# Kernel optimization log

Hardware: AMD Instinct MI355X
Metric: run time of the kernel (lower is better)

The kernel has to match this reference:

```python
import jax, jax.numpy as jnp
import numpy as np

B, KL, XL, DIM, H, PB = 4, 128, 4096, 256, 8, 8
HD = DIM // H
SCALE = HD ** -0.5
N_DIS = 64 + 2


def setup_inputs() -> dict:
    key = jax.random.key(0)
    ks = jax.random.split(key, 10)
    x = jax.random.normal(ks[0], (B, XL, DIM), jnp.float32)
    kernal = jax.random.normal(ks[1], (B, KL, DIM), jnp.float32)
    rd = jax.random.randint(ks[2], (B, KL, XL), 0, N_DIS)
    polar_pos = jax.random.randint(ks[3], (B, KL, XL), 0, PB)
    att_mask = jax.random.uniform(ks[4], (B, H, XL, KL)) < 0.1
    W_qkv = jax.random.normal(ks[5], (DIM, 3 * DIM), jnp.float32) * 0.02
    dis_embed = jax.random.normal(ks[6], (N_DIS, H), jnp.float32) * 0.02
    polar_emb = jax.random.normal(ks[7], (PB, 1), jnp.float32) * 0.02
    W_proj = jax.random.normal(ks[8], (DIM, DIM), jnp.float32) * 0.02
    b_proj = jnp.zeros((DIM,), jnp.float32)
    return dict(x=x, kernal=kernal, rd=rd, polar_pos=polar_pos, att_mask=att_mask,
                W_qkv=W_qkv, dis_embed=dis_embed, polar_emb=polar_emb,
                W_proj=W_proj, b_proj=b_proj)


def _heads(t, h):
    b, n, d = t.shape
    return t.reshape(b, n, h, d // h).transpose(0, 2, 1, 3)  # b h n hd


def reference(x, kernal, rd, polar_pos, att_mask, W_qkv, dis_embed, polar_emb, W_proj, b_proj):
    b, xl, dim = x.shape
    kl = kernal.shape[1]
    h = H
    scale = (dim // h) ** -0.5

    q, k, v = [_heads(t, h) for t in jnp.split(x @ W_qkv, 3, axis=-1)]        # b h xl hd
    k_q, k_k, k_v = [_heads(t, h) for t in jnp.split(kernal @ W_qkv, 3, axis=-1)]  # b h kl hd

    rd_e = dis_embed[rd].transpose(0, 3, 1, 2)  # (b,kl,xl,h) -> (b,h,kl,xl)

    # kernel -> x attention scores
    k_x_attn = jnp.einsum('bhkd,bhxd->bhkx', k_q, k) * scale  # b h kl xl

    # main orientation: one-hot-weighted |attn| reduced over x, argmax over polar bins
    pp = jnp.broadcast_to(polar_pos[:, None], (b, h, kl, xl))  # b h kl xl
    polar_hot = jax.nn.one_hot(pp, PB, dtype=k_x_attn.dtype)   # b h kl xl o
    ori_sum = jnp.einsum('bhkx,bhkxo->bhko', jnp.abs(k_x_attn), polar_hot)
    main_ori = jnp.argmax(ori_sum, axis=-1)                    # b h kl
    new_polar = pp - main_ori[..., None]
    new_polar = jnp.where(new_polar < 0, new_polar + PB, new_polar)
    polar_bias = polar_emb[new_polar, 0]                       # b h kl xl

    mask_k = att_mask.transpose(0, 1, 3, 2)                    # b h kl xl
    k_x_attn = jnp.where(mask_k, jnp.asarray(-1e6, k_x_attn.dtype), k_x_attn)
    attn_k = jax.nn.softmax(k_x_attn + rd_e + polar_bias, axis=-1)
    k_out = jnp.einsum('bhkx,bhxd->bhkd', attn_k, v)
    k_out = k_out.transpose(0, 2, 1, 3).reshape(b, kl, dim) @ W_proj + b_proj

    # x -> kernel attention scores
    x_k_attn = jnp.einsum('bhxd,bhkd->bhxk', q, k_k) * scale   # b h xl kl
    x_k_attn = jnp.where(att_mask, jnp.asarray(-1e9, x_k_attn.dtype), x_k_attn)
    x_k_attn = jax.nn.softmax(x_k_attn + rd_e.transpose(0, 1, 3, 2)
                              + polar_bias.transpose(0, 1, 3, 2), axis=-1)
    x_out = jnp.einsum('bhxk,bhkd->bhxd', x_k_attn, k_v)
    x_out = x_out.transpose(0, 2, 1, 3).reshape(b, xl, dim) @ W_proj + b_proj

    return (x_out, k_out)
```

## Files before the change

kernel.cpp:

```cpp
#include <hip/hip_runtime.h>
#include <hip/hip_bf16.h>

#define B_    4
#define KL_   128
#define XL_   4096
#define DIM_  256
#define H_    8
#define HD_   32
#define PB_   8
#define NDIS_ 66
#define TDIM_ 768
#define SCALE_ 0.17677669529663687f
#define NS_   4
#define XCH_  (XL_ / NS_)
#define NCH2_ 64
#define KC2_  16

#define NB_CVT_  4096
#define NB_PACK_ 2048
#define NB_WQ_   768
#define NB_WP_   256

typedef float v4f __attribute__((ext_vector_type(4)));
typedef short v8s __attribute__((ext_vector_type(8)));

__device__ __forceinline__ unsigned short f2bf(float f) {
    __hip_bfloat16 h = __float2bfloat16(f);
    return __builtin_bit_cast(unsigned short, h);
}
__device__ __forceinline__ float bf2f(unsigned short u) {
    return __bfloat162float(__builtin_bit_cast(__hip_bfloat16, u));
}
__device__ __forceinline__ void cvt_hilo(float v, unsigned short& hi, unsigned short& lo) {
    hi = f2bf(v);
    lo = f2bf(v - bf2f(hi));
}

__global__ __launch_bounds__(256) void preamble(const float* __restrict__ x,
                                                const int* __restrict__ att_mask,
                                                const float* __restrict__ W_qkv,
                                                const float* __restrict__ W_proj,
                                                unsigned short* __restrict__ xh,
                                                unsigned short* __restrict__ xl,
                                                unsigned int* __restrict__ mbits,
                                                unsigned short* __restrict__ wqh,
                                                unsigned short* __restrict__ wql,
                                                unsigned short* __restrict__ wph,
                                                unsigned short* __restrict__ wpl) {
    const int bid = blockIdx.x, tid = threadIdx.x;
    if (bid < NB_CVT_) {
        size_t i = (size_t)bid * 256 + tid;
        float4 v = *(const float4*)&x[i * 4];
        ushort4 h, l;
        cvt_hilo(v.x, h.x, l.x);
        cvt_hilo(v.y, h.y, l.y);
        cvt_hilo(v.z, h.z, l.z);
        cvt_hilo(v.w, h.w, l.w);
        *(ushort4*)&xh[i * 4] = h;
        *(ushort4*)&xl[i * 4] = l;
    } else if (bid < NB_CVT_ + NB_PACK_) {
        size_t wid = (size_t)(bid - NB_CVT_) * 256 + tid;
        const int* src = &att_mask[wid * 32];
        unsigned bits = 0;
#pragma unroll
        for (int i = 0; i < 8; ++i) {
            int4 m4 = *(const int4*)&src[i * 4];
            bits |= (m4.x ? 1u : 0u) << (i * 4 + 0);
            bits |= (m4.y ? 1u : 0u) << (i * 4 + 1);
            bits |= (m4.z ? 1u : 0u) << (i * 4 + 2);
            bits |= (m4.w ? 1u : 0u) << (i * 4 + 3);
        }
        mbits[wid] = bits;
    } else if (bid < NB_CVT_ + NB_PACK_ + NB_WQ_) {
        int n = bid - (NB_CVT_ + NB_PACK_), k = tid;
        float v = W_qkv[(size_t)k * TDIM_ + n];
        unsigned short h, l;
        cvt_hilo(v, h, l);
        wqh[(size_t)n * DIM_ + k] = h;
        wql[(size_t)n * DIM_ + k] = l;
    } else {
        int n = bid - (NB_CVT_ + NB_PACK_ + NB_WQ_), k = tid;
        float v = W_proj[(size_t)k * DIM_ + n];
        unsigned short h, l;
        cvt_hilo(v, h, l);
        wph[(size_t)n * DIM_ + k] = h;
        wpl[(size_t)n * DIM_ + k] = l;
    }
}

__global__ __launch_bounds__(256) void gemm_mfma(const unsigned short* __restrict__ Ah,
                                                 const unsigned short* __restrict__ Al,
                                                 const unsigned short* __restrict__ Bh,
                                                 const unsigned short* __restrict__ Bl,
                                                 float* __restrict__ C,
                                                 const float* __restrict__ bias,
                                                 int M, int N, int K, int mode,
                                                 unsigned short* __restrict__ qh,
                                                 unsigned short* __restrict__ kh,
                                                 unsigned short* __restrict__ kl2,
                                                 float* __restrict__ vx) {
    __shared__ __align__(16) unsigned short Ah_s[128 * 32];
    __shared__ __align__(16) unsigned short Al_s[128 * 32];
    __shared__ __align__(16) unsigned short Bh_s[128 * 32];
    __shared__ __align__(16) unsigned short Bl_s[128 * 32];
    const int tid = threadIdx.x;
    const int w = tid >> 6, lane = tid & 63;
    const int c = lane & 15, q = lane >> 4;
    const int bm = blockIdx.y * 128, bn = blockIdx.x * 128;

    const int lrow = lane >> 2;
    const int lcol = (lane & 3) * 8;

    v4f acc[2][8] = {};
    for (int k0 = 0; k0 < K; k0 += 32) {
        __syncthreads();
#pragma unroll
        for (int i = 0; i < 2; ++i) {
            const int chunk = w * 2 + i;
            const int row = chunk * 16 + lrow;
            const size_t ga = (size_t)(bm + row) * K + k0 + lcol;
            const size_t gb = (size_t)(bn + row) * K + k0 + lcol;
            const int lo = chunk * 512;
            __builtin_amdgcn_global_load_lds(
                (const __attribute__((address_space(1))) unsigned int*)&Ah[ga],
                (__attribute__((address_space(3))) unsigned int*)&Ah_s[lo], 16, 0, 0);
            __builtin_amdgcn_global_load_lds(
                (const __attribute__((address_space(1))) unsigned int*)&Al[ga],
                (__attribute__((address_space(3))) unsigned int*)&Al_s[lo], 16, 0, 0);
            __builtin_amdgcn_global_load_lds(
                (const __attribute__((address_space(1))) unsigned int*)&Bh[gb],
                (__attribute__((address_space(3))) unsigned int*)&Bh_s[lo], 16, 0, 0);
            __builtin_amdgcn_global_load_lds(
                (const __attribute__((address_space(1))) unsigned int*)&Bl[gb],
                (__attribute__((address_space(3))) unsigned int*)&Bl_s[lo], 16, 0, 0);
        }
        asm volatile("s_waitcnt vmcnt(0)" ::: "memory");
        __syncthreads();
        v8s afh[2], afl[2];
#pragma unroll
        for (int mt = 0; mt < 2; ++mt) {
            afh[mt] = *(v8s*)&Ah_s[(w * 32 + mt * 16 + c) * 32 + q * 8];
            afl[mt] = *(v8s*)&Al_s[(w * 32 + mt * 16 + c) * 32 + q * 8];
        }
#pragma unroll
        for (int nt = 0; nt < 8; ++nt) {
            v8s bfh = *(v8s*)&Bh_s[(nt * 16 + c) * 32 + q * 8];
            v8s bfl = *(v8s*)&Bl_s[(nt * 16 + c) * 32 + q * 8];
#pragma unroll
            for (int mt = 0; mt < 2; ++mt) {
                acc[mt][nt] = __builtin_amdgcn_mfma_f32_16x16x32_bf16(afl[mt], bfh, acc[mt][nt], 0, 0, 0);
                acc[mt][nt] = __builtin_amdgcn_mfma_f32_16x16x32_bf16(afh[mt], bfl, acc[mt][nt], 0, 0, 0);
                acc[mt][nt] = __builtin_amdgcn_mfma_f32_16x16x32_bf16(afh[mt], bfh, acc[mt][nt], 0, 0, 0);
            }
        }
    }
    if (mode == 0) {
#pragma unroll
        for (int mt = 0; mt < 2; ++mt) {
#pragma unroll
            for (int nt = 0; nt < 8; ++nt) {
                int col = bn + nt * 16 + c;
                float bv = bias ? bias[col] : 0.0f;
#pragma unroll
                for (int r = 0; r < 4; ++r) {
                    int row = bm + w * 32 + mt * 16 + q * 4 + r;
                    C[(size_t)row * N + col] = acc[mt][nt][r] + bv;
                }
            }
        }
    } else {
#pragma unroll
        for (int mt = 0; mt < 2; ++mt) {
#pragma unroll
            for (int nt = 0; nt < 8; ++nt) {
                int col = bn + nt * 16 + c;
#pragma unroll
                for (int r = 0; r < 4; ++r) {
                    int row = bm + w * 32 + mt * 16 + q * 4 + r;
                    float v = acc[mt][nt][r];
                    if (col < DIM_) {
                        qh[(size_t)row * DIM_ + col] = f2bf(v);
                    } else if (col < 2 * DIM_) {
                        unsigned short hi, lo;
                        cvt_hilo(v, hi, lo);
                        kh[(size_t)row * DIM_ + col - DIM_] = hi;
                        kl2[(size_t)row * DIM_ + col - DIM_] = lo;
                    } else {
                        vx[(size_t)row * DIM_ + col - 2 * DIM_] = v;
                    }
                }
            }
        }
    }
}

__global__ __launch_bounds__(256) void gemm64(const float* __restrict__ A,
                                              const float* __restrict__ Bw,
                                              float* __restrict__ C,
                                              const float* __restrict__ bias,
                                              int M, int N, int K) {
    __shared__ __align__(16) float As[16][68];
    __shared__ __align__(16) float Bs[16][64];
    const int tid = threadIdx.x;
    const int tx = tid & 15, ty = tid >> 4;
    const int bn = blockIdx.x * 64, bm = blockIdx.y * 64;
    const int am = tid >> 2, ac = tid & 3;
    float acc[4][4] = {};
    for (int k0 = 0; k0 < K; k0 += 16) {
        float4 a4 = *(const float4*)&A[(size_t)(bm + am) * K + k0 + ac * 4];
        As[ac * 4 + 0][am] = a4.x;
        As[ac * 4 + 1][am] = a4.y;
        As[ac * 4 + 2][am] = a4.z;
        As[ac * 4 + 3][am] = a4.w;
        *(float4*)&Bs[ty][tx * 4] = *(const float4*)&Bw[(size_t)(k0 + ty) * N + bn + tx * 4];
        __syncthreads();
#pragma unroll
        for (int kk = 0; kk < 16; ++kk) {
            float4 av = *(const float4*)&As[kk][ty * 4];
            float4 bv = *(const float4*)&Bs[kk][tx * 4];
            float a[4] = {av.x, av.y, av.z, av.w};
            float b[4] = {bv.x, bv.y, bv.z, bv.w};
#pragma unroll
            for (int i = 0; i < 4; ++i)
#pragma unroll
                for (int j = 0; j < 4; ++j) acc[i][j] += a[i] * b[j];
        }
        __syncthreads();
    }
#pragma unroll
    for (int i = 0; i < 4; ++i) {
        int m = bm + ty * 4 + i;
#pragma unroll
        for (int j = 0; j < 4; ++j) {
            int n = bn + tx * 4 + j;
            float v = acc[i][j];
            if (bias) v += bias[n];
            C[(size_t)m * N + n] = v;
        }
    }
}

__global__ __launch_bounds__(256) void gemm64_qkv(const float* __restrict__ A,
                                                  const float* __restrict__ Bw,
                                                  unsigned short* __restrict__ Kqh,
                                                  unsigned short* __restrict__ Kql,
                                                  unsigned short* __restrict__ Kk_bf,
                                                  unsigned short* __restrict__ VT_bf,
                                                  int M, int N, int K) {
    __shared__ __align__(16) float As[16][68];
    __shared__ __align__(16) float Bs[16][64];
    const int tid = threadIdx.x;
    const int tx = tid & 15, ty = tid >> 4;
    const int bn = blockIdx.x * 64, bm = blockIdx.y * 64;
    const int am = tid >> 2, ac = tid & 3;
    float acc[4][4] = {};
    for (int k0 = 0; k0 < K; k0 += 16) {
        float4 a4 = *(const float4*)&A[(size_t)(bm + am) * K + k0 + ac * 4];
        As[ac * 4 + 0][am] = a4.x;
        As[ac * 4 + 1][am] = a4.y;
        As[ac * 4 + 2][am] = a4.z;
        As[ac * 4 + 3][am] = a4.w;
        *(float4*)&Bs[ty][tx * 4] = *(const float4*)&Bw[(size_t)(k0 + ty) * N + bn + tx * 4];
        __syncthreads();
#pragma unroll
        for (int kk = 0; kk < 16; ++kk) {
            float4 av = *(const float4*)&As[kk][ty * 4];
            float4 bv = *(const float4*)&Bs[kk][tx * 4];
            float a[4] = {av.x, av.y, av.z, av.w};
            float b[4] = {bv.x, bv.y, bv.z, bv.w};
#pragma unroll
            for (int i = 0; i < 4; ++i)
#pragma unroll
                for (int j = 0; j < 4; ++j) acc[i][j] += a[i] * b[j];
        }
        __syncthreads();
    }
#pragma unroll
    for (int i = 0; i < 4; ++i) {
        int m = bm + ty * 4 + i;
        int b = m >> 7, k = m & 127;
#pragma unroll
        for (int j = 0; j < 4; ++j) {
            int n = bn + tx * 4 + j;
            float v = acc[i][j];
            if (n < DIM_) {
                unsigned short hi, lo;
                cvt_hilo(v, hi, lo);
                int h = n >> 5, d = n & 31;
                size_t o = ((size_t)(b * H_ + h) * KL_ + k) * HD_ + d;
                Kqh[o] = hi;
                Kql[o] = lo;
            } else if (n < 2 * DIM_) {
                int nn = n - DIM_, h = nn >> 5, d = nn & 31;
                Kk_bf[((size_t)(b * H_ + h) * KL_ + k) * HD_ + d] = f2bf(v);
            } else {
                int nn = n - 2 * DIM_, h = nn >> 5, d = nn & 31;
                VT_bf[((size_t)(b * H_ + h) * HD_ + d) * KL_ + k] = f2bf(v);
            }
        }
    }
}

__global__ __launch_bounds__(256) void score_bins_mfma4(const unsigned short* __restrict__ kxh,
                                                        const unsigned short* __restrict__ kxl,
                                                        const unsigned short* __restrict__ Kqh_g,
                                                        const unsigned short* __restrict__ Kql_g,
                                                        const int* __restrict__ rd,
                                                        const int* __restrict__ polar_pos,
                                                        const unsigned int* __restrict__ mbits,
                                                        const float* __restrict__ dis_embed,
                                                        __hip_bfloat16* __restrict__ Sg,
                                                        float* __restrict__ binspart) {
    const int b = blockIdx.z, h = blockIdx.y, xc = blockIdx.x;
    const int x0 = xc * 64;
    const int tid = threadIdx.x;
    const int w = tid >> 6, lane = tid & 63;
    const int c15 = lane & 15, q = lane >> 4;
    const size_t bh = (size_t)(b * H_ + h);

    __shared__ unsigned int mskb[64][5];
    __shared__ float de_h[NDIS_];
    __shared__ float binsL[8][4][16][PB_ + 1];
    __shared__ __align__(16) unsigned short Ss[2][16][72];

    {
        int xr = tid >> 2, kg = tid & 3;
        mskb[xr][kg] = mbits[(bh * XL_ + x0 + xr) * 4 + kg];
    }
    if (tid < NDIS_) de_h[tid] = dis_embed[tid * H_ + h];
    __syncthreads();

    v8s axh, axl;
    {
        const size_t aoff = ((size_t)b * XL_ + x0 + w * 16 + c15) * DIM_ + h * HD_ + q * 8;
        axh = *(const v8s*)&kxh[aoff];
        axl = *(const v8s*)&kxl[aoff];
    }

    v8s bqh[2], bql[2];
    int4 r4[2], p4[2];
    auto load_nt = [&](int nt, int s) {
        const int k = nt * 16 + c15;
        const size_t kqoff = (bh * KL_ + k) * HD_ + q * 8;
        bqh[s] = *(const v8s*)&Kqh_g[kqoff];
        bql[s] = *(const v8s*)&Kql_g[kqoff];
        const size_t rowoff = ((size_t)(b * KL_ + k)) * XL_ + x0 + w * 16 + q * 4;
        r4[s] = *(const int4*)&rd[rowoff];
        p4[s] = *(const int4*)&polar_pos[rowoff];
    };
    load_nt(0, 0);

#pragma unroll
    for (int nt = 0; nt < 8; ++nt) {
        const int s = nt & 1;
        if (nt < 7) load_nt(nt + 1, s ^ 1);

        const int k = nt * 16 + c15;
        v4f D = {0.f, 0.f, 0.f, 0.f};
        D = __builtin_amdgcn_mfma_f32_16x16x32_bf16(axl, bqh[s], D, 0, 0, 0);
        D = __builtin_amdgcn_mfma_f32_16x16x32_bf16(axh, bql[s], D, 0, 0, 0);
        D = __builtin_amdgcn_mfma_f32_16x16x32_bf16(axh, bqh[s], D, 0, 0, 0);

        float bins[PB_] = {};
        {
            int rv[4] = {r4[s].x, r4[s].y, r4[s].z, r4[s].w};
            int pv[4] = {p4[s].x, p4[s].y, p4[s].z, p4[s].w};
            ushort4 pack;
#pragma unroll
            for (int r = 0; r < 4; ++r) {
                float sc = D[r] * SCALE_;
                float a = fabsf(sc);
                int pp = pv[r];
#pragma unroll
                for (int pb = 0; pb < PB_; ++pb) bins[pb] += (pp == pb) ? a : 0.0f;
                int xloc = w * 16 + q * 4 + r;
                int mbit = (mskb[xloc][k >> 5] >> (k & 31)) & 1;
                float sp = (mbit ? -1e6f : sc) + de_h[rv[r]];
                ((unsigned short*)&pack)[r] = f2bf(sp);
            }
            *(ushort4*)&Ss[s][c15][w * 16 + q * 4] = pack;
        }

#pragma unroll
        for (int pb = 0; pb < PB_; ++pb) {
            bins[pb] += __shfl_xor(bins[pb], 16);
            bins[pb] += __shfl_xor(bins[pb], 32);
        }
        if (q == 0) {
#pragma unroll
            for (int pb = 0; pb < PB_; ++pb) binsL[nt][w][c15][pb] = bins[pb];
        }

        __syncthreads();
        {
            int row = tid >> 4, seg = tid & 15;
            unsigned short* dst = (unsigned short*)Sg +
                (bh * KL_ + nt * 16 + row) * XL_ + x0 + seg * 4;
            *(uint2*)dst = *(const uint2*)&Ss[s][row][seg * 4];
        }
    }
    __syncthreads();
    {
        int k = tid >> 1, half = tid & 1;
        int nt = k >> 4, c = k & 15;
        float4 s = {0.f, 0.f, 0.f, 0.f};
#pragma unroll
        for (int w4 = 0; w4 < 4; ++w4) {
            const float* bp = &binsL[nt][w4][c][half * 4];
            s.x += bp[0]; s.y += bp[1]; s.z += bp[2]; s.w += bp[3];
        }
        *(float4*)&binspart[(bh * KL_ + k) * (NCH2_ * PB_) + xc * PB_ + half * 4] = s;
    }
}

__global__ __launch_bounds__(256) void bins_argmax(const float* __restrict__ binspart,
                                                   int* __restrict__ main_ori) {
    const int w = threadIdx.x >> 6, lane = threadIdx.x & 63;
    const int row = blockIdx.x * 4 + w;
    float s[PB_];
#pragma unroll
    for (int pb = 0; pb < PB_; ++pb) s[pb] = 0.0f;
    if (lane < NCH2_) {
        const float* bp = &binspart[(size_t)row * (NCH2_ * PB_) + lane * PB_];
#pragma unroll
        for (int pb = 0; pb < PB_; ++pb) s[pb] = bp[pb];
    }
#pragma unroll
    for (int m = 1; m < 64; m <<= 1)
#pragma unroll
        for (int pb = 0; pb < PB_; ++pb) s[pb] += __shfl_xor(s[pb], m);
    if (lane == 0) {
        float best = s[0];
        int bi = 0;
#pragma unroll
        for (int pb = 1; pb < PB_; ++pb)
            if (s[pb] > best) { best = s[pb]; bi = pb; }
        main_ori[row] = bi;
    }
}

__global__ __launch_bounds__(256) void flash_cached2(const float* __restrict__ vx,
                                                     const __hip_bfloat16* __restrict__ Sg,
                                                     const int* __restrict__ polar_pos,
                                                     const float* __restrict__ polar_emb,
                                                     const int* __restrict__ main_ori,
                                                     float* __restrict__ part) {
    const int b = blockIdx.z, h = blockIdx.y;
    const int kch = blockIdx.x / NS_, xc = blockIdx.x % NS_;
    const int k0 = kch * KC2_;
    const int tid = threadIdx.x;
    const int ki = tid >> 4, xt = tid & 15;

    __shared__ __align__(16) float4 vs[64][9];
    __shared__ int pol_s[KC2_][68];
    __shared__ float pe[PB_];

    if (tid < PB_) pe[tid] = polar_emb[tid];
    const size_t bh = (size_t)(b * H_ + h);
    const size_t row_k = bh * KL_ + k0 + ki;
    const int mo = main_ori[row_k];
    const int xbeg = xc * XCH_;

    float l = 0.f;
    float4 acc[8] = {};
    __syncthreads();
    for (int t = 0; t < XCH_ / 64; ++t) {
        const int x0 = xbeg + t * 64;
        __syncthreads();
#pragma unroll
        for (int i = 0; i < 2; ++i) {
            int id = tid + 256 * i;
            int row = id >> 3, c = id & 7;
            vs[row][c] = *(const float4*)&vx[(size_t)(b * XL_ + x0 + row) * DIM_ + h * HD_ + c * 4];
        }
        {
            int kk = tid >> 4, c = tid & 15;
            *(int4*)&pol_s[kk][c * 4] =
                *(const int4*)&polar_pos[(size_t)(b * KL_ + k0 + kk) * XL_ + x0 + c * 4];
        }
        __syncthreads();
#pragma unroll
        for (int j = 0; j < 4; ++j) {
            int xl = xt + 16 * j;
            int x = x0 + xl;
            float sp = __bfloat162float(Sg[row_k * XL_ + x]);
            int pp = pol_s[ki][xl];
            int np = pp - mo;
            np += (np >> 31) & PB_;
            float p = __expf(sp + pe[np]);
            l += p;
#pragma unroll
            for (int c = 0; c < 8; ++c) {
                float4 v = vs[xl][c];
                acc[c].x += p * v.x; acc[c].y += p * v.y;
                acc[c].z += p * v.z; acc[c].w += p * v.w;
            }
        }
    }
#pragma unroll
    for (int m = 1; m < 16; m <<= 1) {
        l += __shfl_xor(l, m, 16);
#pragma unroll
        for (int c = 0; c < 8; ++c) {
            acc[c].x += __shfl_xor(acc[c].x, m, 16);
            acc[c].y += __shfl_xor(acc[c].y, m, 16);
            acc[c].z += __shfl_xor(acc[c].z, m, 16);
            acc[c].w += __shfl_xor(acc[c].w, m, 16);
        }
    }
    if (xt == 0) {
        float* dst = &part[(size_t)(row_k * NS_ + xc) * 36];
#pragma unroll
        for (int c = 0; c < 8; ++c) *(float4*)&dst[c * 4] = acc[c];
        dst[32] = l;
    }
}

__global__ __launch_bounds__(256) void merge_cached(const float* __restrict__ part,
                                                    float* __restrict__ kout_pre) {
    const int tid = threadIdx.x;
    const int ri = tid >> 5, d = tid & 31;
    const int row = blockIdx.x * 8 + ri;
    float l = 0.f, a = 0.f;
#pragma unroll
    for (int c = 0; c < NS_; ++c) {
        const float* p = &part[(size_t)(row * NS_ + c) * 36];
        l += p[32];
        a += p[d];
    }
    int k = row & (KL_ - 1);
    int bh = row >> 7;
    int h = bh & (H_ - 1), b = bh >> 3;
    kout_pre[(size_t)(b * KL_ + k) * DIM_ + h * HD_ + d] = a / l;
}

__global__ __launch_bounds__(256) void attn_x_mfma(const unsigned short* __restrict__ qxh,
                                                   const unsigned short* __restrict__ Kk_bf,
                                                   const unsigned short* __restrict__ VT_bf,
                                                   const int* __restrict__ rd,
                                                   const int* __restrict__ polar_pos,
                                                   const unsigned int* __restrict__ mbits,
                                                   const float* __restrict__ dis_embed,
                                                   const float* __restrict__ polar_emb,
                                                   const int* __restrict__ main_ori,
                                                   unsigned short* __restrict__ oh,
                                                   unsigned short* __restrict__ ol) {
    const int b = blockIdx.z, h = blockIdx.y;
    const int x0 = blockIdx.x * 64;
    const int tid = threadIdx.x;
    const int wave = tid >> 6, lane = tid & 63;
    const int c = lane & 15, q = lane >> 4;

    __shared__ __align__(16) unsigned short P_s[4][16][136];
    __shared__ unsigned short rp_s[KL_][72];
    __shared__ unsigned int msk_s[64][5];
    __shared__ float de_h[NDIS_];
    __shared__ float pe[PB_];
    __shared__ int mo_s[KL_];

    const size_t bh = (size_t)(b * H_ + h);
    if (tid < NDIS_) de_h[tid] = dis_embed[tid * H_ + h];
    if (tid < PB_) pe[tid] = polar_emb[tid];
    if (tid < KL_) mo_s[tid] = main_ori[bh * KL_ + tid];
    {
        int xr = tid >> 2, kg = tid & 3;
        msk_s[xr][kg] = mbits[(bh * XL_ + x0 + xr) * 4 + kg];
    }
    __syncthreads();

#pragma unroll
    for (int i = 0; i < 8; ++i) {
        int id = tid + 256 * i;
        int k = id >> 4, cc = id & 15;
        size_t gb = (size_t)(b * KL_ + k) * XL_ + x0 + cc * 4;
        int4 r4 = *(const int4*)&rd[gb];
        int4 p4 = *(const int4*)&polar_pos[gb];
        int mo = mo_s[k];
        int n0 = p4.x - mo; n0 += (n0 >> 31) & PB_;
        int n1 = p4.y - mo; n1 += (n1 >> 31) & PB_;
        int n2 = p4.z - mo; n2 += (n2 >> 31) & PB_;
        int n3 = p4.w - mo; n3 += (n3 >> 31) & PB_;
        rp_s[k][cc * 4 + 0] = (unsigned short)(r4.x | (n0 << 8));
        rp_s[k][cc * 4 + 1] = (unsigned short)(r4.y | (n1 << 8));
        rp_s[k][cc * 4 + 2] = (unsigned short)(r4.z | (n2 << 8));
        rp_s[k][cc * 4 + 3] = (unsigned short)(r4.w | (n3 << 8));
    }
    __syncthreads();

    v8s aq = *(const v8s*)&qxh[(size_t)(b * XL_ + x0 + wave * 16 + c) * DIM_ + h * HD_ + q * 8];

    const unsigned short* KkB = &Kk_bf[(size_t)bh * KL_ * HD_];
    v4f S[8];
#pragma unroll
    for (int t = 0; t < 8; ++t) {
        v8s bk = *(const v8s*)&KkB[(size_t)(t * 16 + c) * HD_ + q * 8];
        S[t] = __builtin_amdgcn_mfma_f32_16x16x32_bf16(aq, bk, (v4f){0.f, 0.f, 0.f, 0.f}, 0, 0, 0);
    }

    const int xloc = wave * 16;
    float lr[4] = {0.f, 0.f, 0.f, 0.f};
#pragma unroll
    for (int t = 0; t < 8; ++t) {
#pragma unroll
        for (int r = 0; r < 4; ++r) {
            int krow = t * 16 + c;
            int xrow = q * 4 + r;
            unsigned short rp = rp_s[krow][xloc + xrow];
            int mbit = (msk_s[xloc + xrow][krow >> 5] >> (krow & 31)) & 1;
            float sval = S[t][r] * SCALE_;
            float tval = (mbit ? -25.0f : sval) + de_h[rp & 0x7f] + pe[(rp >> 8) & 7];
            float p = __expf(tval);
            unsigned short pb = f2bf(p);
            P_s[wave][xrow][krow] = pb;
            lr[r] += bf2f(pb);
        }
    }
#pragma unroll
    for (int r = 0; r < 4; ++r) {
#pragma unroll
        for (int m = 1; m < 16; m <<= 1) lr[r] += __shfl_xor(lr[r], m);
    }
    __syncthreads();

    const unsigned short* VTB = &VT_bf[(size_t)bh * HD_ * KL_];
    v4f O0 = {0.f, 0.f, 0.f, 0.f}, O1 = {0.f, 0.f, 0.f, 0.f};
#pragma unroll
    for (int kc = 0; kc < 4; ++kc) {
        v8s ap = *(v8s*)&P_s[wave][c][kc * 32 + q * 8];
        v8s bv0 = *(const v8s*)&VTB[(size_t)c * KL_ + kc * 32 + q * 8];
        v8s bv1 = *(const v8s*)&VTB[(size_t)(16 + c) * KL_ + kc * 32 + q * 8];
        O0 = __builtin_amdgcn_mfma_f32_16x16x32_bf16(ap, bv0, O0, 0, 0, 0);
        O1 = __builtin_amdgcn_mfma_f32_16x16x32_bf16(ap, bv1, O1, 0, 0, 0);
    }

#pragma unroll
    for (int r = 0; r < 4; ++r) {
        int xg = x0 + wave * 16 + q * 4 + r;
        float inv = 1.0f / lr[r];
        size_t obase = (size_t)(b * XL_ + xg) * DIM_ + h * HD_;
        float v0 = O0[r] * inv;
        float v1 = O1[r] * inv;
        unsigned short h0, l0, h1, l1;
        cvt_hilo(v0, h0, l0);
        cvt_hilo(v1, h1, l1);
        oh[obase + c] = h0;
        ol[obase + c] = l0;
        oh[obase + 16 + c] = h1;
        ol[obase + 16 + c] = l1;
    }
}

extern "C" void kernel_launch(void* const* d_in, const int* in_sizes, int n_in,
                              void* d_out, int out_size, void* d_ws, size_t ws_size,
                              hipStream_t stream) {
    const float* x         = (const float*)d_in[0];
    const float* kernal    = (const float*)d_in[1];
    const int* rd          = (const int*)d_in[2];
    const int* polar_pos   = (const int*)d_in[3];
    const int* att_mask    = (const int*)d_in[4];
    const float* W_qkv     = (const float*)d_in[5];
    const float* dis_embed = (const float*)d_in[6];
    const float* polar_emb = (const float*)d_in[7];
    const float* W_proj    = (const float*)d_in[8];
    const float* b_proj    = (const float*)d_in[9];
    float* out             = (float*)d_out;

    char* base = (char*)d_ws;
    size_t off = 0;
    auto alloc = [&](size_t bytes) { void* p = base + off; off = (off + bytes + 255) & ~255ULL; return p; };
    const size_t MX = (size_t)B_ * XL_;

    float* vx        = (float*)alloc(MX * DIM_ * 4);
    unsigned short* qxh = (unsigned short*)alloc(MX * DIM_ * 2);
    unsigned short* kxh = (unsigned short*)alloc(MX * DIM_ * 2);
    unsigned short* kxl = (unsigned short*)alloc(MX * DIM_ * 2);
    float* binspart  = (float*)alloc((size_t)B_ * H_ * KL_ * NCH2_ * PB_ * 4);
    float* kout_pre  = (float*)alloc((size_t)B_ * KL_ * DIM_ * 4);
    int* main_ori    = (int*)alloc(B_ * H_ * KL_ * 4);
    float* part      = (float*)alloc((size_t)B_ * H_ * KL_ * NS_ * 36 * 4);
    __hip_bfloat16* Sg = (__hip_bfloat16*)alloc((size_t)B_ * H_ * KL_ * XL_ * 2);
    unsigned short* wph = (unsigned short*)alloc((size_t)DIM_ * DIM_ * 2);
    unsigned short* wpl = (unsigned short*)alloc((size_t)DIM_ * DIM_ * 2);
    unsigned short* wqh = (unsigned short*)alloc((size_t)TDIM_ * DIM_ * 2);
    unsigned short* wql = (unsigned short*)alloc((size_t)TDIM_ * DIM_ * 2);
    unsigned int* mbits = (unsigned int*)alloc((size_t)B_ * H_ * XL_ * (KL_ / 32) * 4);
    unsigned short* Kqh_g = (unsigned short*)alloc((size_t)B_ * H_ * KL_ * HD_ * 2);
    unsigned short* Kql_g = (unsigned short*)alloc((size_t)B_ * H_ * KL_ * HD_ * 2);
    unsigned short* Kk_bf = (unsigned short*)alloc((size_t)B_ * H_ * KL_ * HD_ * 2);
    unsigned short* VT_bf = (unsigned short*)alloc((size_t)B_ * H_ * HD_ * KL_ * 2);

    unsigned short* xh = (unsigned short*)Sg;
    unsigned short* xl_ = xh + MX * DIM_;
    unsigned short* oh = (unsigned short*)Sg;
    unsigned short* ol = oh + MX * DIM_;

    preamble<<<dim3(NB_CVT_ + NB_PACK_ + NB_WQ_ + NB_WP_), 256, 0, stream>>>(
        x, att_mask, W_qkv, W_proj, xh, xl_, mbits, wqh, wql, wph, wpl);

    gemm_mfma<<<dim3(TDIM_ / 128, MX / 128), 256, 0, stream>>>(
        xh, xl_, wqh, wql, nullptr, nullptr, MX, TDIM_, DIM_, 1, qxh, kxh, kxl, vx);
    gemm64_qkv<<<dim3(TDIM_ / 64, (B_ * KL_) / 64), 256, 0, stream>>>(
        kernal, W_qkv, Kqh_g, Kql_g, Kk_bf, VT_bf, B_ * KL_, TDIM_, DIM_);

    score_bins_mfma4<<<dim3(NCH2_, H_, B_), 256, 0, stream>>>(
        kxh, kxl, Kqh_g, Kql_g, rd, polar_pos, mbits, dis_embed, Sg, binspart);
    bins_argmax<<<dim3(B_ * H_ * KL_ / 4), 256, 0, stream>>>(binspart, main_ori);
    flash_cached2<<<dim3((KL_ / KC2_) * NS_, H_, B_), 256, 0, stream>>>(
        vx, Sg, polar_pos, polar_emb, main_ori, part);
    merge_cached<<<dim3(B_ * H_ * KL_ / 8), 256, 0, stream>>>(part, kout_pre);

    attn_x_mfma<<<dim3(XL_ / 64, H_, B_), 256, 0, stream>>>(
        qxh, Kk_bf, VT_bf, rd, polar_pos, mbits, dis_embed, polar_emb, main_ori, oh, ol);

    gemm_mfma<<<dim3(DIM_ / 128, MX / 128), 256, 0, stream>>>(
        oh, ol, wph, wpl, out, b_proj, MX, DIM_, DIM_, 0, nullptr, nullptr, nullptr, nullptr);
    gemm64<<<dim3(DIM_ / 64, (B_ * KL_) / 64), 256, 0, stream>>>(
        kout_pre, W_proj, out + (size_t)B_ * XL_ * DIM_, b_proj, B_ * KL_, DIM_, DIM_);
}
```

Measured before the change: 335.7 us.

## Stage QKV GEMM epilogue through LDS for vectorized bf16 stores and remap blocks per XCD

The bf16 outputs of the QKV projection GEMM (q, and k split into high and low parts) are now staged through a padded LDS scratch tile so each thread writes 16-byte vectors instead of scattered 2-byte stores. The block-column range also selects the epilogue branch directly, where before every element tested its column. The grid becomes one-dimensional with a remap that keeps consecutive row tiles on the same XCD, aiming at better L2 reuse of shared operands. This adds extra barriers and LDS traffic to the epilogue.

```diff
diff --git a/kernel.cpp b/kernel.cpp
--- a/kernel.cpp
+++ b/kernel.cpp
@@ -15,6 +15,7 @@
 #define XCH_  (XL_ / NS_)
 #define NCH2_ 64
 #define KC2_  16
+#define GM_PITCH_ 132
 
 #define NB_CVT_  4096
 #define NB_PACK_ 2048
@@ -99,14 +100,22 @@
                                                  unsigned short* __restrict__ kh,
                                                  unsigned short* __restrict__ kl2,
                                                  float* __restrict__ vx) {
-    __shared__ __align__(16) unsigned short Ah_s[128 * 32];
-    __shared__ __align__(16) unsigned short Al_s[128 * 32];
-    __shared__ __align__(16) unsigned short Bh_s[128 * 32];
-    __shared__ __align__(16) unsigned short Bl_s[128 * 32];
+    __shared__ __align__(16) char SMEM[64 * GM_PITCH_ * 4];
+    unsigned short* Ah_s = (unsigned short*)SMEM;
+    unsigned short* Al_s = Ah_s + 4096;
+    unsigned short* Bh_s = Ah_s + 8192;
+    unsigned short* Bl_s = Ah_s + 12288;
+    float* scratch = (float*)SMEM;
+
     const int tid = threadIdx.x;
     const int w = tid >> 6, lane = tid & 63;
     const int c = lane & 15, q = lane >> 4;
-    const int bm = blockIdx.y * 128, bn = blockIdx.x * 128;
+
+    const int NBX = N >> 7;
+    const int id = blockIdx.x;
+    const int xcd = id & 7, grp = id >> 3;
+    const int bm = ((grp / NBX) * 8 + xcd) * 128;
+    const int bn = (grp % NBX) * 128;
 
     const int lrow = lane >> 2;
     const int lcol = (lane & 3) * 8;
@@ -168,27 +177,50 @@
                 }
             }
         }
-    } else {
+    } else if (bn >= 2 * DIM_) {
 #pragma unroll
         for (int mt = 0; mt < 2; ++mt) {
 #pragma unroll
             for (int nt = 0; nt < 8; ++nt) {
-                int col = bn + nt * 16 + c;
+                int col = bn + nt * 16 + c - 2 * DIM_;
 #pragma unroll
                 for (int r = 0; r < 4; ++r) {
                     int row = bm + w * 32 + mt * 16 + q * 4 + r;
-                    float v = acc[mt][nt][r];
-                    if (col < DIM_) {
-                        qh[(size_t)row * DIM_ + col] = f2bf(v);
-                    } else if (col < 2 * DIM_) {
-                        unsigned short hi, lo;
-                        cvt_hilo(v, hi, lo);
-                        kh[(size_t)row * DIM_ + col - DIM_] = hi;
-                        kl2[(size_t)row * DIM_ + col - DIM_] = lo;
-                    } else {
-                        vx[(size_t)row * DIM_ + col - 2 * DIM_] = v;
-                    }
+                    vx[(size_t)row * DIM_ + col] = acc[mt][nt][r];
                 }
+            }
+        }
+    } else {
+        for (int mt = 0; mt < 2; ++mt) {
+            __syncthreads();
+#pragma unroll
+            for (int nt = 0; nt < 8; ++nt)
+#pragma unroll
+                for (int r = 0; r < 4; ++r)
+                    scratch[(w * 16 + q * 4 + r) * GM_PITCH_ + nt * 16 + c] = acc[mt][nt][r];
+            __syncthreads();
+            const int or_ = tid & 63, oc = (tid >> 6) * 32;
+            const int grow = bm + (or_ >> 4) * 32 + mt * 16 + (or_ & 15);
+            const float* src = &scratch[or_ * GM_PITCH_ + oc];
+            if (bn < DIM_) {
+                unsigned short tmp[32];
+#pragma unroll
+                for (int j = 0; j < 32; ++j) tmp[j] = f2bf(src[j]);
+                unsigned short* dst = &qh[(size_t)grow * DIM_ + bn + oc];
+#pragma unroll
+                for (int j4 = 0; j4 < 4; ++j4)
+                    *(uint4*)&dst[j4 * 8] = *(uint4*)&tmp[j4 * 8];
+            } else {
+                unsigned short th[32], tl[32];
+#pragma unroll
+                for (int j = 0; j < 32; ++j) cvt_hilo(src[j], th[j], tl[j]);
+                const size_t o = (size_t)grow * DIM_ + bn - DIM_ + oc;
+#pragma unroll
+                for (int j4 = 0; j4 < 4; ++j4)
+                    *(uint4*)&kh[o + j4 * 8] = *(uint4*)&th[j4 * 8];
+#pragma unroll
+                for (int j4 = 0; j4 < 4; ++j4)
+                    *(uint4*)&kl2[o + j4 * 8] = *(uint4*)&tl[j4 * 8];
             }
         }
     }
@@ -697,7 +729,7 @@
     preamble<<<dim3(NB_CVT_ + NB_PACK_ + NB_WQ_ + NB_WP_), 256, 0, stream>>>(
         x, att_mask, W_qkv, W_proj, xh, xl_, mbits, wqh, wql, wph, wpl);
 
-    gemm_mfma<<<dim3(TDIM_ / 128, MX / 128), 256, 0, stream>>>(
+    gemm_mfma<<<dim3((TDIM_ / 128) * (MX / 128)), 256, 0, stream>>>(
         xh, xl_, wqh, wql, nullptr, nullptr, MX, TDIM_, DIM_, 1, qxh, kxh, kxl, vx);
     gemm64_qkv<<<dim3(TDIM_ / 64, (B_ * KL_) / 64), 256, 0, stream>>>(
         kernal, W_qkv, Kqh_g, Kql_g, Kk_bf, VT_bf, B_ * KL_, TDIM_, DIM_);
@@ -712,7 +744,7 @@
     attn_x_mfma<<<dim3(XL_ / 64, H_, B_), 256, 0, stream>>>(
         qxh, Kk_bf, VT_bf, rd, polar_pos, mbits, dis_embed, polar_emb, main_ori, oh, ol);
 
-    gemm_mfma<<<dim3(DIM_ / 128, MX / 128), 256, 0, stream>>>(
+    gemm_mfma<<<dim3((DIM_ / 128) * (MX / 128)), 256, 0, stream>>>(
         oh, ol, wph, wpl, out, b_proj, MX, DIM_, DIM_, 0, nullptr, nullptr, nullptr, nullptr);
     gemm64<<<dim3(DIM_ / 64, (B_ * KL_) / 64), 256, 0, stream>>>(
         kout_pre, W_proj, out + (size_t)B_ * XL_ * DIM_, b_proj, B_ * KL_, DIM_, DIM_);
```

Result: no change. 337.8 us (+0.6%).
